# Optimization experiments

Measured on AMD Instinct MI355X. Metric: run time of the kernel, lower is better.

Reference implementation:

```python
import jax, jax.numpy as jnp
import numpy as np

B, T, N, C = 32, 12, 1024, 2   # batch, lookback window, n_series, in_channels
D, H, K, OUT = 16, 64, 2, 12   # embedding_dim, rnn_units, cheb_k, out_dim (horizon)


def setup_inputs() -> dict:
    key = jax.random.key(0)
    ks = jax.random.split(key, 12)
    p = lambda k, sh, s=0.1: jax.random.normal(k, sh, dtype=jnp.float32) * s
    return {
        "source": jax.random.normal(ks[0], (B, T, N, C), dtype=jnp.float32),
        "node_emb": p(ks[1], (N, D), 0.3),
        # layer 0: dim_in = C + H
        "gate_w0": p(ks[2], (D, K, C + H, 2 * H)),
        "gate_b0": p(ks[3], (D, 2 * H)),
        "upd_w0": p(ks[4], (D, K, C + H, H)),
        "upd_b0": p(ks[5], (D, H)),
        # layer 1: dim_in = H + H
        "gate_w1": p(ks[6], (D, K, 2 * H, 2 * H)),
        "gate_b1": p(ks[7], (D, 2 * H)),
        "upd_w1": p(ks[8], (D, K, 2 * H, H)),
        "upd_b1": p(ks[9], (D, H)),
        # end_conv: Conv2d(1, OUT*out_channels, kernel=(1,H)) == linear over hidden dim
        "conv_w": p(ks[10], (OUT, H)),
        "conv_b": p(ks[11], (OUT,)),
    }


def _supports(node_emb):
    # softmax(relu(E E^T)) row-normalized adaptive adjacency; Chebyshev stack (K, N, N)
    A = jax.nn.softmax(jax.nn.relu(node_emb @ node_emb.T), axis=1)
    s = [jnp.eye(N, dtype=A.dtype), A]
    for _ in range(2, K):
        s.append(2.0 * A @ s[-1] - s[-2])
    return jnp.stack(s, axis=0)


def _gcn(x, node_emb, w_pool, b_pool, supports):
    # x: (B, N, Cin); per-node adaptive weights from pools
    w = jnp.einsum('nd,dkio->nkio', node_emb, w_pool)     # (N, K, Cin, Cout)
    b = node_emb @ b_pool                                 # (N, Cout)
    xg = jnp.einsum('knm,bmc->bnkc', supports, x)         # (B, N, K, Cin)
    return jnp.einsum('bnki,nkio->bno', xg, w) + b


def _layer(x_seq, node_emb, supports, gw, gb, uw, ub):
    # x_seq: (B, T, N, Cin) -> (B, T, N, H) via GRU-style AGCRN cell, scanned over T
    def step(state, x_t):
        inp = jnp.concatenate([x_t, state], axis=-1)
        zr = jax.nn.sigmoid(_gcn(inp, node_emb, gw, gb, supports))
        z, r = jnp.split(zr, 2, axis=-1)
        cand = jnp.concatenate([x_t, z * state], axis=-1)
        hc = jnp.tanh(_gcn(cand, node_emb, uw, ub, supports))
        h = r * state + (1.0 - r) * hc
        return h, h

    init = jnp.zeros((x_seq.shape[0], N, H), dtype=x_seq.dtype)
    _, hs = jax.lax.scan(step, init, jnp.swapaxes(x_seq, 0, 1))
    return jnp.swapaxes(hs, 0, 1)


def reference(source, node_emb, gate_w0, gate_b0, upd_w0, upd_b0,
              gate_w1, gate_b1, upd_w1, upd_b1, conv_w, conv_b,
              teacher_forcing_ratio=0):
    sup = _supports(node_emb)  # adaptive supports depend only on static node_emb
    h1 = _layer(source, node_emb, sup, gate_w0, gate_b0, upd_w0, upd_b0)
    h2 = _layer(h1, node_emb, sup, gate_w1, gate_b1, upd_w1, upd_b1)
    last = h2[:, -1]  # (B, N, H)
    # end_conv over hidden dim -> (B, OUT, N); out_channels==1 so squeeze folds away
    out = jnp.einsum('bnh,oh->bon', last, conv_w) + conv_b[None, :, None]
    return out
```

## Files before the change

kernel.cpp:

```cpp
#include <hip/hip_runtime.h>
#include <hip/hip_fp16.h>


typedef _Float16 f16x8 __attribute__((ext_vector_type(8)));
typedef _Float16 f16x4 __attribute__((ext_vector_type(4)));
typedef float f32x4 __attribute__((ext_vector_type(4)));

__global__ __launch_bounds__(256) void compute_A_kernel(const float* __restrict__ E,
                                                        __half* __restrict__ Ah) {
  int n = blockIdx.x;
  int tid = threadIdx.x;
  __shared__ float red[256];
  float en[16];
#pragma unroll
  for (int d = 0; d < 16; ++d) en[d] = E[n * 16 + d];
  float v[4];
#pragma unroll
  for (int q = 0; q < 4; ++q) {
    int m = tid + q * 256;
    const float* Em = E + m * 16;
    float dot = 0.f;
#pragma unroll
    for (int d = 0; d < 16; ++d) dot += en[d] * Em[d];
    v[q] = fmaxf(dot, 0.f);
  }
  float mx = fmaxf(fmaxf(v[0], v[1]), fmaxf(v[2], v[3]));
  red[tid] = mx; __syncthreads();
  for (int s = 128; s > 0; s >>= 1) { if (tid < s) red[tid] = fmaxf(red[tid], red[tid + s]); __syncthreads(); }
  mx = red[0];
  __syncthreads();
  float e[4], sum = 0.f;
#pragma unroll
  for (int q = 0; q < 4; ++q) { e[q] = expf(v[q] - mx); sum += e[q]; }
  red[tid] = sum; __syncthreads();
  for (int s = 128; s > 0; s >>= 1) { if (tid < s) red[tid] += red[tid + s]; __syncthreads(); }
  float inv = 1.f / red[0];
#pragma unroll
  for (int q = 0; q < 4; ++q) Ah[(size_t)n * 1024 + tid + q * 256] = __float2half(e[q] * inv);
}

__global__ void build_e16_kernel(const float* __restrict__ E, __half* __restrict__ E16) {
  int t = blockIdx.x * 256 + threadIdx.x;
  if (t >= 1024 * 32) return;
  int d = t & 31;
  E16[t] = (d < 16) ? __float2half(E[(t >> 5) * 16 + d]) : __half(0);
}

__global__ void pool_t16_kernel(const float* __restrict__ gw0, const float* __restrict__ uw0,
                                const float* __restrict__ gw1, const float* __restrict__ uw1,
                                __half* __restrict__ poolT16) {
  int t = blockIdx.x * 256 + threadIdx.x;
  if (t >= 79872 * 32) return;
  int d = t & 31, j = t >> 5;
  if (d >= 16) { poolT16[t] = __half(0); return; }
  const float* pool; int F, Fp, O, loc;
  if (j < 20480)      { pool = gw0; F = 66;  Fp = 80;  O = 128; loc = j; }
  else if (j < 30720) { pool = uw0; F = 66;  Fp = 80;  O = 64;  loc = j - 20480; }
  else if (j < 63488) { pool = gw1; F = 128; Fp = 128; O = 128; loc = j - 30720; }
  else                { pool = uw1; F = 128; Fp = 128; O = 64;  loc = j - 63488; }
  int KIp = 2 * Fp;
  int o = loc / KIp, kip = loc - o * KIp;
  int kk = (kip >= Fp) ? 1 : 0;
  int jj = kip - kk * Fp;
  int i;
  if (F == Fp) i = jj;
  else i = (jj < 64) ? jj + 2 : (jj < 66 ? jj - 64 : -1);
  poolT16[t] = (i >= 0) ? __float2half(pool[(((size_t)d * 2 + kk) * F + i) * O + o]) : __half(0);
}

__global__ __launch_bounds__(256) void make_wt_mfma_kernel(
    const __half* __restrict__ E16g, const __half* __restrict__ poolT16g,
    __half* __restrict__ WtG0, __half* __restrict__ WtU0,
    __half* __restrict__ WtG1, __half* __restrict__ WtU1) {
  __shared__ __align__(16) _Float16 Es[64][40];
  __shared__ __align__(16) _Float16 wbuf[64][264];
  const _Float16* E16 = (const _Float16*)E16g;
  const _Float16* pT = (const _Float16*)poolT16g;
  int bx = blockIdx.x;
  __half* Wt; int OK, jbase;
  if (bx < 80)       { Wt = WtG0; OK = 128 * 160; jbase = bx * 256; }
  else if (bx < 120) { Wt = WtU0; OK = 64 * 160;  jbase = (bx - 80) * 256; }
  else if (bx < 248) { Wt = WtG1; OK = 128 * 256; jbase = (bx - 120) * 256; }
  else               { Wt = WtU1; OK = 64 * 256;  jbase = (bx - 248) * 256; }
  int jglob0 = bx * 256;
  int n0 = blockIdx.y * 64;
  {
    int r = threadIdx.x >> 2, ch = (threadIdx.x & 3) * 8;
    *(f16x8*)&Es[r][ch] = *(const f16x8*)(E16 + (size_t)(n0 + r) * 32 + ch);
  }
  __syncthreads();
  int wave = threadIdx.x >> 6, lane = threadIdx.x & 63;
  int fm = lane & 15, fg = lane >> 4;
  f16x8 af[4];
#pragma unroll
  for (int i = 0; i < 4; ++i) af[i] = *(const f16x8*)&Es[i * 16 + fm][fg * 8];
  f32x4 acc[4][4] = {};
#pragma unroll
  for (int j = 0; j < 4; ++j) {
    int jc = jglob0 + wave * 64 + j * 16 + fm;
    f16x8 bf = *(const f16x8*)(pT + (size_t)jc * 32 + fg * 8);
#pragma unroll
    for (int i = 0; i < 4; ++i)
      acc[i][j] = __builtin_amdgcn_mfma_f32_16x16x32_f16(af[i], bf, acc[i][j], 0, 0, 0);
  }
#pragma unroll
  for (int i = 0; i < 4; ++i)
#pragma unroll
    for (int j = 0; j < 4; ++j)
#pragma unroll
      for (int r = 0; r < 4; ++r)
        wbuf[i * 16 + fg * 4 + r][wave * 64 + j * 16 + fm] = (_Float16)acc[i][j][r];
  __syncthreads();
  for (int idx = threadIdx.x; idx < 64 * 32; idx += 256) {
    int nsub = idx >> 5, pos = (idx & 31) * 8;
    *(float4*)(Wt + (size_t)(n0 + nsub) * OK + jbase + pos) = *(float4*)&wbuf[nsub][pos];
  }
}

__global__ void make_b_all_kernel(const float* __restrict__ E,
                                  const float* __restrict__ gb0, const float* __restrict__ ub0,
                                  const float* __restrict__ gb1, const float* __restrict__ ub1,
                                  float* __restrict__ Bg0, float* __restrict__ Bu0,
                                  float* __restrict__ Bg1, float* __restrict__ Bu1) {
  int tid = blockIdx.x * 256 + threadIdx.x;
  if (tid >= 1024 * 384) return;
  int n = tid / 384, c = tid - n * 384;
  const float* pool; float* outp; int O, o;
  if (c < 128)      { pool = gb0; outp = Bg0; O = 128; o = c; }
  else if (c < 192) { pool = ub0; outp = Bu0; O = 64;  o = c - 128; }
  else if (c < 320) { pool = gb1; outp = Bg1; O = 128; o = c - 192; }
  else              { pool = ub1; outp = Bu1; O = 64;  o = c - 320; }
  const float* En = E + n * 16;
  float a = 0.f;
#pragma unroll
  for (int d = 0; d < 16; ++d) a += En[d] * pool[d * O + o];
  outp[n * O + o] = a;
}

__global__ void zero_kernel(float* __restrict__ p, int count) {
  int i = blockIdx.x * 256 + threadIdx.x;
  if (i < count) p[i] = 0.f;
}

__global__ void build_x16_kernel(const float* __restrict__ src, __half* __restrict__ x16) {
  int bid = blockIdx.x; int t = bid >> 5, b = bid & 31;
  const float* s = src + (size_t)(b * 12 + t) * 2048;
  __half* dst = x16 + t * 64 + b * 2;
  for (int n = threadIdx.x; n < 1024; n += 256) {
    float2 v = *(const float2*)(s + n * 2);
    *(__half2*)(dst + (size_t)n * 768) = __floats2half2_rn(v.x, v.y);
  }
}

__global__ __launch_bounds__(256) void gemm_nt_kernel(
    const __half* __restrict__ Ahg, const __half* __restrict__ X0g,
    const __half* __restrict__ X1g, __half* __restrict__ Yg,
    int Nc, int cstride, int split) {
  __shared__ __align__(16) _Float16 As[64][136];
  __shared__ __align__(16) _Float16 Bs[64][144];
  const _Float16* __restrict__ Ah = (const _Float16*)Ahg;
  _Float16* __restrict__ Y = (_Float16*)Yg;
  int tid = threadIdx.x;
  int row0 = blockIdx.y * 64;
  int col0 = blockIdx.x * 64;
  const _Float16* __restrict__ Xsrc =
      (col0 < split) ? (const _Float16*)X0g : (const _Float16*)X1g;
  int colg = (col0 < split) ? col0 : col0 - split;
  int wave = tid >> 6, lane = tid & 63;
  int wm = wave & 1, wn = wave >> 1;
  int fm = lane & 15, fg = lane >> 4;

  int sr = tid >> 2, sc = (tid & 3) * 32;
  const _Float16* pa = Ah + (size_t)(row0 + sr) * 1024 + sc;
  int kq = tid & 31, cg = tid >> 5;
  int kb = 4 * kq;
  const _Float16* pb = Xsrc + (size_t)kb * cstride + colg + cg * 8;
  int chunk = kq >> 1;
  int kin = (kq & 1) * 4;

  f16x8 ra[4], rb[4];
#pragma unroll
  for (int c = 0; c < 4; ++c) ra[c] = *(const f16x8*)(pa + c * 8);
#pragma unroll
  for (int r = 0; r < 4; ++r) rb[r] = *(const f16x8*)(pb + (size_t)r * cstride);

  f32x4 acc[2][2] = {};
  for (int k0 = 0; k0 < 1024; k0 += 128) {
#pragma unroll
    for (int c = 0; c < 4; ++c) *(f16x8*)&As[sr][sc + c * 8] = ra[c];
#pragma unroll
    for (int i = 0; i < 8; ++i) {
      int c = cg * 8 + i;
      f16x4 p;
      p[0] = rb[0][i]; p[1] = rb[1][i]; p[2] = rb[2][i]; p[3] = rb[3][i];
      *(f16x4*)&Bs[c][((chunk ^ (c & 7)) << 3) + kin] = p;
    }
    __syncthreads();
    if (k0 + 128 < 1024) {
#pragma unroll
      for (int c = 0; c < 4; ++c) ra[c] = *(const f16x8*)(pa + k0 + 128 + c * 8);
#pragma unroll
      for (int r = 0; r < 4; ++r)
        rb[r] = *(const f16x8*)(pb + (size_t)(k0 + 128 + r) * cstride);
    }
#pragma unroll
    for (int kc = 0; kc < 4; ++kc) {
      int ck = kc * 4 + fg;
      f16x8 af[2], bf[2];
#pragma unroll
      for (int i = 0; i < 2; ++i)
        af[i] = *(const f16x8*)&As[wm * 32 + i * 16 + fm][kc * 32 + fg * 8];
#pragma unroll
      for (int j = 0; j < 2; ++j) {
        int cl = wn * 32 + j * 16 + fm;
        bf[j] = *(const f16x8*)&Bs[cl][(ck ^ (cl & 7)) << 3];
      }
#pragma unroll
      for (int i = 0; i < 2; ++i)
#pragma unroll
        for (int j = 0; j < 2; ++j)
          acc[i][j] = __builtin_amdgcn_mfma_f32_16x16x32_f16(af[i], bf[j], acc[i][j], 0, 0, 0);
    }
    __syncthreads();
  }
#pragma unroll
  for (int i = 0; i < 2; ++i) {
#pragma unroll
    for (int j = 0; j < 2; ++j) {
      int col = col0 + wn * 32 + j * 16 + fm;
      int rbase = row0 + wm * 32 + i * 16 + fg * 4;
#pragma unroll
      for (int r = 0; r < 4; ++r)
        Y[(size_t)(rbase + r) * Nc + col] = (_Float16)acc[i][j][r];
    }
  }
}

__global__ __launch_bounds__(256) void gate0_kernel(
    const __half* __restrict__ h16, const __half* __restrict__ YB,
    const float* __restrict__ src, const __half* __restrict__ Axt, int tstep,
    const __half* __restrict__ Wtg, const float* __restrict__ Bg,
    const float* __restrict__ h32, __half* __restrict__ zh, float* __restrict__ rbuf) {
  constexpr int KIP = 160, STRIDE = 168;
  __shared__ __align__(16) _Float16 Xs[32 * STRIDE];
  int n = blockIdx.x;
  int t = threadIdx.x;
#pragma unroll
  for (int u = 0; u < 2; ++u) {
    int idx = t + u * 256;
    int b = idx >> 4, part = (idx >> 3) & 1, ch = idx & 7;
    const _Float16* s = part ? (const _Float16*)YB + (size_t)n * 2048 + b * 64 + ch * 8
                             : (const _Float16*)h16 + (size_t)n * 2048 + b * 64 + ch * 8;
    *(f16x8*)&Xs[b * STRIDE + part * 80 + ch * 8] = *(const f16x8*)s;
  }
  if (t < 32) {
    int b = t;
    float2 xv = *(const float2*)(src + ((size_t)(b * 12 + tstep) * 1024 + n) * 2);
    Xs[b * STRIDE + 64] = (_Float16)xv.x;
    Xs[b * STRIDE + 65] = (_Float16)xv.y;
    const _Float16* ax = (const _Float16*)Axt + (size_t)n * 768 + tstep * 64 + b * 2;
    Xs[b * STRIDE + 144] = ax[0];
    Xs[b * STRIDE + 145] = ax[1];
  }
  for (int idx = t; idx < 896; idx += 256) {
    int b = idx / 28, jj = idx % 28;
    int col = (jj < 14) ? 66 + jj : 132 + jj;
    Xs[b * STRIDE + col] = (_Float16)0.f;
  }
  __syncthreads();
  int wave = t >> 6, lane = t & 63;
  int fm = lane & 15, fg = lane >> 4;
  f32x4 acc[2][2] = {};
  const _Float16* Wn = (const _Float16*)Wtg + ((size_t)n * 128 + wave * 32) * KIP;
#pragma unroll
  for (int kc = 0; kc < KIP / 32; ++kc) {
    f16x8 af[2], bf[2];
#pragma unroll
    for (int i = 0; i < 2; ++i)
      af[i] = *(const f16x8*)&Xs[(i * 16 + fm) * STRIDE + kc * 32 + fg * 8];
#pragma unroll
    for (int j = 0; j < 2; ++j)
      bf[j] = *(const f16x8*)(Wn + (size_t)(j * 16 + fm) * KIP + kc * 32 + fg * 8);
#pragma unroll
    for (int i = 0; i < 2; ++i)
#pragma unroll
      for (int j = 0; j < 2; ++j)
        acc[i][j] = __builtin_amdgcn_mfma_f32_16x16x32_f16(af[i], bf[j], acc[i][j], 0, 0, 0);
  }
  const float* Bn = Bg + n * 128;
#pragma unroll
  for (int j = 0; j < 2; ++j) {
    int o = wave * 32 + j * 16 + fm;
    float bias = Bn[o];
#pragma unroll
    for (int i = 0; i < 2; ++i)
#pragma unroll
      for (int r = 0; r < 4; ++r) {
        int b = i * 16 + fg * 4 + r;
        float s = 1.f / (1.f + __expf(-(acc[i][j][r] + bias)));
        size_t base = (size_t)n * 2048 + b * 64;
        if (o < 64) zh[base + o] = __float2half(s * h32[base + o]);
        else        rbuf[base + o - 64] = s;
      }
  }
}

__global__ __launch_bounds__(256) void upd0_kernel(
    const __half* __restrict__ zh, const __half* __restrict__ YA2,
    const float* __restrict__ src, const __half* __restrict__ Axt, int tstep,
    const __half* __restrict__ Wtg, const float* __restrict__ Bu,
    const float* __restrict__ rbuf, float* __restrict__ h32, __half* __restrict__ h16) {
  constexpr int KIP = 160, STRIDE = 168;
  __shared__ __align__(16) _Float16 Xs[32 * STRIDE];
  int n = blockIdx.x;
  int t = threadIdx.x;
#pragma unroll
  for (int u = 0; u < 2; ++u) {
    int idx = t + u * 256;
    int b = idx >> 4, part = (idx >> 3) & 1, ch = idx & 7;
    const _Float16* s = part ? (const _Float16*)YA2 + (size_t)n * 4096 + b * 64 + ch * 8
                             : (const _Float16*)zh + (size_t)n * 2048 + b * 64 + ch * 8;
    *(f16x8*)&Xs[b * STRIDE + part * 80 + ch * 8] = *(const f16x8*)s;
  }
  if (t < 32) {
    int b = t;
    float2 xv = *(const float2*)(src + ((size_t)(b * 12 + tstep) * 1024 + n) * 2);
    Xs[b * STRIDE + 64] = (_Float16)xv.x;
    Xs[b * STRIDE + 65] = (_Float16)xv.y;
    const _Float16* ax = (const _Float16*)Axt + (size_t)n * 768 + tstep * 64 + b * 2;
    Xs[b * STRIDE + 144] = ax[0];
    Xs[b * STRIDE + 145] = ax[1];
  }
  for (int idx = t; idx < 896; idx += 256) {
    int b = idx / 28, jj = idx % 28;
    int col = (jj < 14) ? 66 + jj : 132 + jj;
    Xs[b * STRIDE + col] = (_Float16)0.f;
  }
  __syncthreads();
  int wave = t >> 6, lane = t & 63;
  int fm = lane & 15, fg = lane >> 4;
  f32x4 acc[2] = {};
  const _Float16* Wn = (const _Float16*)Wtg + ((size_t)n * 64 + wave * 16) * KIP;
#pragma unroll
  for (int kc = 0; kc < KIP / 32; ++kc) {
    f16x8 bf = *(const f16x8*)(Wn + (size_t)fm * KIP + kc * 32 + fg * 8);
#pragma unroll
    for (int i = 0; i < 2; ++i) {
      f16x8 af = *(const f16x8*)&Xs[(i * 16 + fm) * STRIDE + kc * 32 + fg * 8];
      acc[i] = __builtin_amdgcn_mfma_f32_16x16x32_f16(af, bf, acc[i], 0, 0, 0);
    }
  }
  int o = wave * 16 + fm;
  float bias = Bu[n * 64 + o];
#pragma unroll
  for (int i = 0; i < 2; ++i)
#pragma unroll
    for (int r = 0; r < 4; ++r) {
      int b = i * 16 + fg * 4 + r;
      float x = acc[i][r] + bias;
      x = fminf(fmaxf(x, -15.f), 15.f);
      float e = __expf(2.f * x);
      float hc = (e - 1.f) / (e + 1.f);
      size_t base = (size_t)n * 2048 + b * 64;
      float rr = rbuf[base + o];
      float hnew = rr * h32[base + o] + (1.f - rr) * hc;
      h32[base + o] = hnew;
      h16[base + o] = __float2half(hnew);
    }
}

__global__ __launch_bounds__(256) void gate1_kernel(
    const __half* __restrict__ h1_16, const __half* __restrict__ h2_16,
    const __half* __restrict__ YB, const __half* __restrict__ YA2,
    const __half* __restrict__ Wtg, const float* __restrict__ Bg,
    const float* __restrict__ h32, __half* __restrict__ zh, float* __restrict__ rbuf) {
  constexpr int KIP = 256, STRIDE = 264;
  __shared__ __align__(16) _Float16 Xs[32 * STRIDE];
  int n = blockIdx.x;
  int t = threadIdx.x;
#pragma unroll
  for (int u = 0; u < 4; ++u) {
    int idx = t + u * 256;
    int b = idx >> 5, q = idx & 31;
    const _Float16* s;
    if (q < 8)       s = (const _Float16*)h1_16 + (size_t)n * 2048 + b * 64 + q * 8;
    else if (q < 16) s = (const _Float16*)h2_16 + (size_t)n * 2048 + b * 64 + (q - 8) * 8;
    else if (q < 24) s = (const _Float16*)YB + (size_t)n * 2048 + b * 64 + (q - 16) * 8;
    else             s = (const _Float16*)YA2 + (size_t)n * 4096 + 2048 + b * 64 + (q - 24) * 8;
    *(f16x8*)&Xs[b * STRIDE + q * 8] = *(const f16x8*)s;
  }
  __syncthreads();
  int wave = t >> 6, lane = t & 63;
  int fm = lane & 15, fg = lane >> 4;
  f32x4 acc[2][2] = {};
  const _Float16* Wn = (const _Float16*)Wtg + ((size_t)n * 128 + wave * 32) * KIP;
#pragma unroll
  for (int kc = 0; kc < KIP / 32; ++kc) {
    f16x8 af[2], bf[2];
#pragma unroll
    for (int i = 0; i < 2; ++i)
      af[i] = *(const f16x8*)&Xs[(i * 16 + fm) * STRIDE + kc * 32 + fg * 8];
#pragma unroll
    for (int j = 0; j < 2; ++j)
      bf[j] = *(const f16x8*)(Wn + (size_t)(j * 16 + fm) * KIP + kc * 32 + fg * 8);
#pragma unroll
    for (int i = 0; i < 2; ++i)
#pragma unroll
      for (int j = 0; j < 2; ++j)
        acc[i][j] = __builtin_amdgcn_mfma_f32_16x16x32_f16(af[i], bf[j], acc[i][j], 0, 0, 0);
  }
  const float* Bn = Bg + n * 128;
#pragma unroll
  for (int j = 0; j < 2; ++j) {
    int o = wave * 32 + j * 16 + fm;
    float bias = Bn[o];
#pragma unroll
    for (int i = 0; i < 2; ++i)
#pragma unroll
      for (int r = 0; r < 4; ++r) {
        int b = i * 16 + fg * 4 + r;
        float s = 1.f / (1.f + __expf(-(acc[i][j][r] + bias)));
        size_t base = (size_t)n * 2048 + b * 64;
        if (o < 64) zh[base + o] = __float2half(s * h32[base + o]);
        else        rbuf[base + o - 64] = s;
      }
  }
}

__global__ __launch_bounds__(256) void upd1_kernel(
    const __half* __restrict__ h1_16, const __half* __restrict__ zh,
    const __half* __restrict__ YB, const __half* __restrict__ YC,
    const __half* __restrict__ Wtg, const float* __restrict__ Bu,
    const float* __restrict__ rbuf, float* __restrict__ h32, __half* __restrict__ h16) {
  constexpr int KIP = 256, STRIDE = 264;
  __shared__ __align__(16) _Float16 Xs[32 * STRIDE];
  int n = blockIdx.x;
  int t = threadIdx.x;
#pragma unroll
  for (int u = 0; u < 4; ++u) {
    int idx = t + u * 256;
    int b = idx >> 5, q = idx & 31;
    const _Float16* s;
    if (q < 8)       s = (const _Float16*)h1_16 + (size_t)n * 2048 + b * 64 + q * 8;
    else if (q < 16) s = (const _Float16*)zh + (size_t)n * 2048 + b * 64 + (q - 8) * 8;
    else if (q < 24) s = (const _Float16*)YB + (size_t)n * 2048 + b * 64 + (q - 16) * 8;
    else             s = (const _Float16*)YC + (size_t)n * 2048 + b * 64 + (q - 24) * 8;
    *(f16x8*)&Xs[b * STRIDE + q * 8] = *(const f16x8*)s;
  }
  __syncthreads();
  int wave = t >> 6, lane = t & 63;
  int fm = lane & 15, fg = lane >> 4;
  f32x4 acc[2] = {};
  const _Float16* Wn = (const _Float16*)Wtg + ((size_t)n * 64 + wave * 16) * KIP;
#pragma unroll
  for (int kc = 0; kc < KIP / 32; ++kc) {
    f16x8 bf = *(const f16x8*)(Wn + (size_t)fm * KIP + kc * 32 + fg * 8);
#pragma unroll
    for (int i = 0; i < 2; ++i) {
      f16x8 af = *(const f16x8*)&Xs[(i * 16 + fm) * STRIDE + kc * 32 + fg * 8];
      acc[i] = __builtin_amdgcn_mfma_f32_16x16x32_f16(af, bf, acc[i], 0, 0, 0);
    }
  }
  int o = wave * 16 + fm;
  float bias = Bu[n * 64 + o];
#pragma unroll
  for (int i = 0; i < 2; ++i)
#pragma unroll
    for (int r = 0; r < 4; ++r) {
      int b = i * 16 + fg * 4 + r;
      float x = acc[i][r] + bias;
      x = fminf(fmaxf(x, -15.f), 15.f);
      float e = __expf(2.f * x);
      float hc = (e - 1.f) / (e + 1.f);
      size_t base = (size_t)n * 2048 + b * 64;
      float rr = rbuf[base + o];
      float hnew = rr * h32[base + o] + (1.f - rr) * hc;
      h32[base + o] = hnew;
      h16[base + o] = __float2half(hnew);
    }
}

__global__ void final_conv_kernel(const float* __restrict__ h2, const float* __restrict__ cw,
                                  const float* __restrict__ cb, float* __restrict__ out) {
  int tid = blockIdx.x * 256 + threadIdx.x;
  if (tid >= 32 * 1024) return;
  int n = tid & 1023, b = tid >> 10;
  const float* hp = h2 + ((size_t)n * 32 + b) * 64;
  float hv[64];
#pragma unroll
  for (int i = 0; i < 64; ++i) hv[i] = hp[i];
#pragma unroll
  for (int o = 0; o < 12; ++o) {
    float acc = cb[o];
#pragma unroll
    for (int i = 0; i < 64; ++i) acc += hv[i] * cw[o * 64 + i];
    out[((size_t)b * 12 + o) * 1024 + n] = acc;
  }
}

extern "C" void kernel_launch(void* const* d_in, const int* in_sizes, int n_in,
                              void* d_out, int out_size, void* d_ws, size_t ws_size,
                              hipStream_t stream) {
  const float* src = (const float*)d_in[0];
  const float* E   = (const float*)d_in[1];
  const float* gw0 = (const float*)d_in[2];
  const float* gb0 = (const float*)d_in[3];
  const float* uw0 = (const float*)d_in[4];
  const float* ub0 = (const float*)d_in[5];
  const float* gw1 = (const float*)d_in[6];
  const float* gb1 = (const float*)d_in[7];
  const float* uw1 = (const float*)d_in[8];
  const float* ub1 = (const float*)d_in[9];
  const float* cw  = (const float*)d_in[10];
  const float* cb  = (const float*)d_in[11];
  float* out = (float*)d_out;
  (void)in_sizes; (void)n_in; (void)out_size; (void)ws_size;

  char* base = (char*)d_ws;
  size_t off = 0;
  auto alloc = [&](size_t bytes) -> void* {
    void* p = base + off; off += (bytes + 511) & ~(size_t)511; return p;
  };
  __half* Ah   = (__half*)alloc((size_t)1024 * 1024 * 2);
  __half* WtG0 = (__half*)alloc((size_t)1024 * 128 * 160 * 2);
  __half* WtU0 = (__half*)alloc((size_t)1024 * 64 * 160 * 2);
  __half* WtG1 = (__half*)alloc((size_t)1024 * 128 * 256 * 2);
  __half* WtU1 = (__half*)alloc((size_t)1024 * 64 * 256 * 2);
  float*  Bg0  = (float*) alloc((size_t)1024 * 128 * 4);
  float*  Bu0  = (float*) alloc((size_t)1024 * 64 * 4);
  float*  Bg1  = (float*) alloc((size_t)1024 * 128 * 4);
  float*  Bu1  = (float*) alloc((size_t)1024 * 64 * 4);
  float*  h1_32 = (float*)alloc((size_t)1024 * 2048 * 4);
  float*  h2_32 = (float*)alloc((size_t)1024 * 2048 * 4);
  __half* h1_16 = (__half*)alloc((size_t)1024 * 2048 * 2);
  __half* h2_16 = (__half*)alloc((size_t)1024 * 2048 * 2);
  __half* YB   = (__half*)alloc((size_t)1024 * 2048 * 2);
  __half* zh   = (__half*)alloc((size_t)1024 * 2048 * 2);
  __half* YA2  = (__half*)alloc((size_t)1024 * 4096 * 2);
  __half* YC   = (__half*)alloc((size_t)1024 * 2048 * 2);
  __half* Axt  = (__half*)alloc((size_t)1024 * 768 * 2);
  float*  rbuf = (float*) alloc((size_t)1024 * 2048 * 4);
  __half* poolT16 = (__half*)rbuf;
  __half* E16  = poolT16 + (size_t)79872 * 32;
  __half* x16  = E16 + (size_t)1024 * 32;

  compute_A_kernel<<<1024, 256, 0, stream>>>(E, Ah);
  build_e16_kernel<<<(1024 * 32 + 255) / 256, 256, 0, stream>>>(E, E16);
  pool_t16_kernel<<<(79872 * 32 + 255) / 256, 256, 0, stream>>>(gw0, uw0, gw1, uw1, poolT16);
  make_wt_mfma_kernel<<<dim3(312, 16), 256, 0, stream>>>(E16, poolT16, WtG0, WtU0, WtG1, WtU1);
  make_b_all_kernel<<<(1024 * 384 + 255) / 256, 256, 0, stream>>>(E, gb0, ub0, gb1, ub1,
                                                                  Bg0, Bu0, Bg1, Bu1);
  build_x16_kernel<<<384, 256, 0, stream>>>(src, x16);
  gemm_nt_kernel<<<dim3(12, 16), 256, 0, stream>>>(Ah, (__half*)x16, (__half*)x16, Axt,
                                                   768, 768, 768);
  zero_kernel<<<(7340032 + 255) / 256, 256, 0, stream>>>(h1_32, 7340032);

  for (int t = 0; t < 12; ++t) {
    gate0_kernel<<<1024, 256, 0, stream>>>(h1_16, YB, src, Axt, t, WtG0, Bg0, h1_32, zh, rbuf);
    gemm_nt_kernel<<<dim3(64, 16), 256, 0, stream>>>(Ah, zh, h2_16, YA2, 4096, 2048, 2048);
    upd0_kernel<<<1024, 256, 0, stream>>>(zh, YA2, src, Axt, t, WtU0, Bu0, rbuf, h1_32, h1_16);
    gemm_nt_kernel<<<dim3(32, 16), 256, 0, stream>>>(Ah, h1_16, h1_16, YB, 2048, 2048, 2048);
    gate1_kernel<<<1024, 256, 0, stream>>>(h1_16, h2_16, YB, YA2, WtG1, Bg1, h2_32, zh, rbuf);
    gemm_nt_kernel<<<dim3(32, 16), 256, 0, stream>>>(Ah, zh, zh, YC, 2048, 2048, 2048);
    upd1_kernel<<<1024, 256, 0, stream>>>(h1_16, zh, YB, YC, WtU1, Bu1, rbuf, h2_32, h2_16);
  }

  final_conv_kernel<<<(32 * 1024 + 255) / 256, 256, 0, stream>>>(h2_32, cw, cb, out);
}
```

Measured before the change: 1.516 ms.

## Fuse next-step layer-0 gate into layer-1 update; add 64x128-tile support GEMM

Layer-0's gate computation for step t+1 now runs inside the layer-1 update kernel of step t. This drops one kernel launch per timestep and reuses the per-node block's shared memory. Separate zh/r buffers are introduced for the two layers so the fused gate cannot clobber state that is still in use. The large 4096-column support GEMM now uses a new kernel with 64x128 tiles, a register prefetch of the next K slice and a swizzled B layout in LDS, halving the grid. The trade-off is higher register and LDS pressure per block, plus extra buffers.

```diff
diff --git a/kernel.cpp b/kernel.cpp
--- a/kernel.cpp
+++ b/kernel.cpp
@@ -236,15 +236,103 @@
   }
 }
 
-__global__ __launch_bounds__(256) void gate0_kernel(
+__global__ __launch_bounds__(256) void gemm_nt128_kernel(
+    const __half* __restrict__ Ahg, const __half* __restrict__ X0g,
+    const __half* __restrict__ X1g, __half* __restrict__ Yg,
+    int Nc, int cstride, int split) {
+  __shared__ __align__(16) _Float16 As[64][136];
+  __shared__ __align__(16) _Float16 Bs[128][144];
+  const _Float16* __restrict__ Ah = (const _Float16*)Ahg;
+  _Float16* __restrict__ Y = (_Float16*)Yg;
+  int tid = threadIdx.x;
+  int row0 = blockIdx.y * 64;
+  int col0 = blockIdx.x * 128;
+  const _Float16* __restrict__ Xsrc =
+      (col0 < split) ? (const _Float16*)X0g : (const _Float16*)X1g;
+  int colg = (col0 < split) ? col0 : col0 - split;
+  int wave = tid >> 6, lane = tid & 63;
+  int fm = lane & 15, fg = lane >> 4;
+
+  int sr = tid >> 2, sc = (tid & 3) * 32;
+  const _Float16* pa = Ah + (size_t)(row0 + sr) * 1024 + sc;
+  int kq = tid & 31, cg = tid >> 5;
+  int kb = 4 * kq;
+  const _Float16* pb = Xsrc + (size_t)kb * cstride + colg + cg * 16;
+  int chunk = kq >> 1;
+  int kin = (kq & 1) * 4;
+
+  f16x8 ra[4], rb[4][2];
+#pragma unroll
+  for (int c = 0; c < 4; ++c) ra[c] = *(const f16x8*)(pa + c * 8);
+#pragma unroll
+  for (int r = 0; r < 4; ++r)
+#pragma unroll
+    for (int h = 0; h < 2; ++h)
+      rb[r][h] = *(const f16x8*)(pb + (size_t)r * cstride + h * 8);
+
+  f32x4 acc[4][2] = {};
+  for (int k0 = 0; k0 < 1024; k0 += 128) {
+#pragma unroll
+    for (int c = 0; c < 4; ++c) *(f16x8*)&As[sr][sc + c * 8] = ra[c];
+#pragma unroll
+    for (int h = 0; h < 2; ++h)
+#pragma unroll
+      for (int i = 0; i < 8; ++i) {
+        int c = cg * 16 + h * 8 + i;
+        f16x4 p;
+        p[0] = rb[0][h][i]; p[1] = rb[1][h][i]; p[2] = rb[2][h][i]; p[3] = rb[3][h][i];
+        *(f16x4*)&Bs[c][((chunk ^ (c & 7)) << 3) + kin] = p;
+      }
+    __syncthreads();
+    if (k0 + 128 < 1024) {
+#pragma unroll
+      for (int c = 0; c < 4; ++c) ra[c] = *(const f16x8*)(pa + k0 + 128 + c * 8);
+#pragma unroll
+      for (int r = 0; r < 4; ++r)
+#pragma unroll
+        for (int h = 0; h < 2; ++h)
+          rb[r][h] = *(const f16x8*)(pb + (size_t)(k0 + 128 + r) * cstride + h * 8);
+    }
+#pragma unroll
+    for (int kc = 0; kc < 4; ++kc) {
+      int ck = kc * 4 + fg;
+      f16x8 af[4], bf[2];
+#pragma unroll
+      for (int i = 0; i < 4; ++i)
+        af[i] = *(const f16x8*)&As[i * 16 + fm][kc * 32 + fg * 8];
+#pragma unroll
+      for (int j = 0; j < 2; ++j) {
+        int cl = wave * 32 + j * 16 + fm;
+        bf[j] = *(const f16x8*)&Bs[cl][(ck ^ (cl & 7)) << 3];
+      }
+#pragma unroll
+      for (int i = 0; i < 4; ++i)
+#pragma unroll
+        for (int j = 0; j < 2; ++j)
+          acc[i][j] = __builtin_amdgcn_mfma_f32_16x16x32_f16(af[i], bf[j], acc[i][j], 0, 0, 0);
+    }
+    __syncthreads();
+  }
+#pragma unroll
+  for (int i = 0; i < 4; ++i) {
+#pragma unroll
+    for (int j = 0; j < 2; ++j) {
+      int col = col0 + wave * 32 + j * 16 + fm;
+      int rbase = row0 + i * 16 + fg * 4;
+#pragma unroll
+      for (int r = 0; r < 4; ++r)
+        Y[(size_t)(rbase + r) * Nc + col] = (_Float16)acc[i][j][r];
+    }
+  }
+}
+
+__device__ __forceinline__ void gate0_body(
+    _Float16* Xs, int n, int t,
     const __half* __restrict__ h16, const __half* __restrict__ YB,
     const float* __restrict__ src, const __half* __restrict__ Axt, int tstep,
     const __half* __restrict__ Wtg, const float* __restrict__ Bg,
-    const float* __restrict__ h32, __half* __restrict__ zh, float* __restrict__ rbuf) {
+    const float* __restrict__ h32, __half* __restrict__ zh0, float* __restrict__ r0) {
   constexpr int KIP = 160, STRIDE = 168;
-  __shared__ __align__(16) _Float16 Xs[32 * STRIDE];
-  int n = blockIdx.x;
-  int t = threadIdx.x;
 #pragma unroll
   for (int u = 0; u < 2; ++u) {
     int idx = t + u * 256;
@@ -299,17 +387,26 @@
         int b = i * 16 + fg * 4 + r;
         float s = 1.f / (1.f + __expf(-(acc[i][j][r] + bias)));
         size_t base = (size_t)n * 2048 + b * 64;
-        if (o < 64) zh[base + o] = __float2half(s * h32[base + o]);
-        else        rbuf[base + o - 64] = s;
+        if (o < 64) zh0[base + o] = __float2half(s * h32[base + o]);
+        else        r0[base + o - 64] = s;
       }
   }
 }
 
+__global__ __launch_bounds__(256) void gate0_kernel(
+    const __half* __restrict__ h16, const __half* __restrict__ YB,
+    const float* __restrict__ src, const __half* __restrict__ Axt, int tstep,
+    const __half* __restrict__ Wtg, const float* __restrict__ Bg,
+    const float* __restrict__ h32, __half* __restrict__ zh0, float* __restrict__ r0) {
+  __shared__ __align__(16) _Float16 Xs[32 * 168];
+  gate0_body(Xs, blockIdx.x, threadIdx.x, h16, YB, src, Axt, tstep, Wtg, Bg, h32, zh0, r0);
+}
+
 __global__ __launch_bounds__(256) void upd0_kernel(
-    const __half* __restrict__ zh, const __half* __restrict__ YA2,
+    const __half* __restrict__ zh0, const __half* __restrict__ YA2,
     const float* __restrict__ src, const __half* __restrict__ Axt, int tstep,
     const __half* __restrict__ Wtg, const float* __restrict__ Bu,
-    const float* __restrict__ rbuf, float* __restrict__ h32, __half* __restrict__ h16) {
+    const float* __restrict__ r0, float* __restrict__ h32, __half* __restrict__ h16) {
   constexpr int KIP = 160, STRIDE = 168;
   __shared__ __align__(16) _Float16 Xs[32 * STRIDE];
   int n = blockIdx.x;
@@ -319,7 +416,7 @@
     int idx = t + u * 256;
     int b = idx >> 4, part = (idx >> 3) & 1, ch = idx & 7;
     const _Float16* s = part ? (const _Float16*)YA2 + (size_t)n * 4096 + b * 64 + ch * 8
-                             : (const _Float16*)zh + (size_t)n * 2048 + b * 64 + ch * 8;
+                             : (const _Float16*)zh0 + (size_t)n * 2048 + b * 64 + ch * 8;
     *(f16x8*)&Xs[b * STRIDE + part * 80 + ch * 8] = *(const f16x8*)s;
   }
   if (t < 32) {
@@ -362,7 +459,7 @@
       float e = __expf(2.f * x);
       float hc = (e - 1.f) / (e + 1.f);
       size_t base = (size_t)n * 2048 + b * 64;
-      float rr = rbuf[base + o];
+      float rr = r0[base + o];
       float hnew = rr * h32[base + o] + (1.f - rr) * hc;
       h32[base + o] = hnew;
       h16[base + o] = __float2half(hnew);
@@ -373,7 +470,7 @@
     const __half* __restrict__ h1_16, const __half* __restrict__ h2_16,
     const __half* __restrict__ YB, const __half* __restrict__ YA2,
     const __half* __restrict__ Wtg, const float* __restrict__ Bg,
-    const float* __restrict__ h32, __half* __restrict__ zh, float* __restrict__ rbuf) {
+    const float* __restrict__ h32, __half* __restrict__ zh1, float* __restrict__ r1) {
   constexpr int KIP = 256, STRIDE = 264;
   __shared__ __align__(16) _Float16 Xs[32 * STRIDE];
   int n = blockIdx.x;
@@ -421,17 +518,21 @@
         int b = i * 16 + fg * 4 + r;
         float s = 1.f / (1.f + __expf(-(acc[i][j][r] + bias)));
         size_t base = (size_t)n * 2048 + b * 64;
-        if (o < 64) zh[base + o] = __float2half(s * h32[base + o]);
-        else        rbuf[base + o - 64] = s;
+        if (o < 64) zh1[base + o] = __float2half(s * h32[base + o]);
+        else        r1[base + o - 64] = s;
       }
   }
 }
 
-__global__ __launch_bounds__(256) void upd1_kernel(
-    const __half* __restrict__ h1_16, const __half* __restrict__ zh,
+__global__ __launch_bounds__(256) void upd1_gate0_kernel(
+    const __half* __restrict__ h1_16, const __half* __restrict__ zh1,
     const __half* __restrict__ YB, const __half* __restrict__ YC,
-    const __half* __restrict__ Wtg, const float* __restrict__ Bu,
-    const float* __restrict__ rbuf, float* __restrict__ h32, __half* __restrict__ h16) {
+    const __half* __restrict__ WtU1, const float* __restrict__ Bu1,
+    const float* __restrict__ r1, float* __restrict__ h2_32, __half* __restrict__ h2_16,
+    const float* __restrict__ src, const __half* __restrict__ Axt, int tnext,
+    const __half* __restrict__ WtG0, const float* __restrict__ Bg0,
+    const float* __restrict__ h1_32, __half* __restrict__ zh0, float* __restrict__ r0,
+    int do_gate0) {
   constexpr int KIP = 256, STRIDE = 264;
   __shared__ __align__(16) _Float16 Xs[32 * STRIDE];
   int n = blockIdx.x;
@@ -442,7 +543,7 @@
     int b = idx >> 5, q = idx & 31;
     const _Float16* s;
     if (q < 8)       s = (const _Float16*)h1_16 + (size_t)n * 2048 + b * 64 + q * 8;
-    else if (q < 16) s = (const _Float16*)zh + (size_t)n * 2048 + b * 64 + (q - 8) * 8;
+    else if (q < 16) s = (const _Float16*)zh1 + (size_t)n * 2048 + b * 64 + (q - 8) * 8;
     else if (q < 24) s = (const _Float16*)YB + (size_t)n * 2048 + b * 64 + (q - 16) * 8;
     else             s = (const _Float16*)YC + (size_t)n * 2048 + b * 64 + (q - 24) * 8;
     *(f16x8*)&Xs[b * STRIDE + q * 8] = *(const f16x8*)s;
@@ -450,34 +551,39 @@
   __syncthreads();
   int wave = t >> 6, lane = t & 63;
   int fm = lane & 15, fg = lane >> 4;
-  f32x4 acc[2] = {};
-  const _Float16* Wn = (const _Float16*)Wtg + ((size_t)n * 64 + wave * 16) * KIP;
-#pragma unroll
-  for (int kc = 0; kc < KIP / 32; ++kc) {
-    f16x8 bf = *(const f16x8*)(Wn + (size_t)fm * KIP + kc * 32 + fg * 8);
-#pragma unroll
-    for (int i = 0; i < 2; ++i) {
-      f16x8 af = *(const f16x8*)&Xs[(i * 16 + fm) * STRIDE + kc * 32 + fg * 8];
-      acc[i] = __builtin_amdgcn_mfma_f32_16x16x32_f16(af, bf, acc[i], 0, 0, 0);
-    }
-  }
-  int o = wave * 16 + fm;
-  float bias = Bu[n * 64 + o];
-#pragma unroll
-  for (int i = 0; i < 2; ++i)
-#pragma unroll
-    for (int r = 0; r < 4; ++r) {
-      int b = i * 16 + fg * 4 + r;
-      float x = acc[i][r] + bias;
-      x = fminf(fmaxf(x, -15.f), 15.f);
-      float e = __expf(2.f * x);
-      float hc = (e - 1.f) / (e + 1.f);
-      size_t base = (size_t)n * 2048 + b * 64;
-      float rr = rbuf[base + o];
-      float hnew = rr * h32[base + o] + (1.f - rr) * hc;
-      h32[base + o] = hnew;
-      h16[base + o] = __float2half(hnew);
-    }
+  {
+    f32x4 acc[2] = {};
+    const _Float16* Wn = (const _Float16*)WtU1 + ((size_t)n * 64 + wave * 16) * KIP;
+#pragma unroll
+    for (int kc = 0; kc < KIP / 32; ++kc) {
+      f16x8 bf = *(const f16x8*)(Wn + (size_t)fm * KIP + kc * 32 + fg * 8);
+#pragma unroll
+      for (int i = 0; i < 2; ++i) {
+        f16x8 af = *(const f16x8*)&Xs[(i * 16 + fm) * STRIDE + kc * 32 + fg * 8];
+        acc[i] = __builtin_amdgcn_mfma_f32_16x16x32_f16(af, bf, acc[i], 0, 0, 0);
+      }
+    }
+    int o = wave * 16 + fm;
+    float bias = Bu1[n * 64 + o];
+#pragma unroll
+    for (int i = 0; i < 2; ++i)
+#pragma unroll
+      for (int r = 0; r < 4; ++r) {
+        int b = i * 16 + fg * 4 + r;
+        float x = acc[i][r] + bias;
+        x = fminf(fmaxf(x, -15.f), 15.f);
+        float e = __expf(2.f * x);
+        float hc = (e - 1.f) / (e + 1.f);
+        size_t base = (size_t)n * 2048 + b * 64;
+        float rr = r1[base + o];
+        float hnew = rr * h2_32[base + o] + (1.f - rr) * hc;
+        h2_32[base + o] = hnew;
+        h2_16[base + o] = __float2half(hnew);
+      }
+  }
+  if (!do_gate0) return;
+  __syncthreads();
+  gate0_body(Xs, n, t, h1_16, YB, src, Axt, tnext, WtG0, Bg0, h1_32, zh0, r0);
 }
 
 __global__ void final_conv_kernel(const float* __restrict__ h2, const float* __restrict__ cw,
@@ -535,12 +641,14 @@
   __half* h1_16 = (__half*)alloc((size_t)1024 * 2048 * 2);
   __half* h2_16 = (__half*)alloc((size_t)1024 * 2048 * 2);
   __half* YB   = (__half*)alloc((size_t)1024 * 2048 * 2);
-  __half* zh   = (__half*)alloc((size_t)1024 * 2048 * 2);
+  __half* zh0  = (__half*)alloc((size_t)1024 * 2048 * 2);
+  __half* zh1  = (__half*)alloc((size_t)1024 * 2048 * 2);
   __half* YA2  = (__half*)alloc((size_t)1024 * 4096 * 2);
   __half* YC   = (__half*)alloc((size_t)1024 * 2048 * 2);
   __half* Axt  = (__half*)alloc((size_t)1024 * 768 * 2);
-  float*  rbuf = (float*) alloc((size_t)1024 * 2048 * 4);
-  __half* poolT16 = (__half*)rbuf;
+  float*  r1   = (float*) alloc((size_t)1024 * 2048 * 4);
+  float*  r0   = (float*) alloc((size_t)1024 * 2048 * 4);
+  __half* poolT16 = (__half*)r0;
   __half* E16  = poolT16 + (size_t)79872 * 32;
   __half* x16  = E16 + (size_t)1024 * 32;
 
@@ -554,15 +662,17 @@
   gemm_nt_kernel<<<dim3(12, 16), 256, 0, stream>>>(Ah, (__half*)x16, (__half*)x16, Axt,
                                                    768, 768, 768);
   zero_kernel<<<(7340032 + 255) / 256, 256, 0, stream>>>(h1_32, 7340032);
+  gate0_kernel<<<1024, 256, 0, stream>>>(h1_16, YB, src, Axt, 0, WtG0, Bg0, h1_32, zh0, r0);
 
   for (int t = 0; t < 12; ++t) {
-    gate0_kernel<<<1024, 256, 0, stream>>>(h1_16, YB, src, Axt, t, WtG0, Bg0, h1_32, zh, rbuf);
-    gemm_nt_kernel<<<dim3(64, 16), 256, 0, stream>>>(Ah, zh, h2_16, YA2, 4096, 2048, 2048);
-    upd0_kernel<<<1024, 256, 0, stream>>>(zh, YA2, src, Axt, t, WtU0, Bu0, rbuf, h1_32, h1_16);
+    gemm_nt128_kernel<<<dim3(32, 16), 256, 0, stream>>>(Ah, zh0, h2_16, YA2, 4096, 2048, 2048);
+    upd0_kernel<<<1024, 256, 0, stream>>>(zh0, YA2, src, Axt, t, WtU0, Bu0, r0, h1_32, h1_16);
     gemm_nt_kernel<<<dim3(32, 16), 256, 0, stream>>>(Ah, h1_16, h1_16, YB, 2048, 2048, 2048);
-    gate1_kernel<<<1024, 256, 0, stream>>>(h1_16, h2_16, YB, YA2, WtG1, Bg1, h2_32, zh, rbuf);
-    gemm_nt_kernel<<<dim3(32, 16), 256, 0, stream>>>(Ah, zh, zh, YC, 2048, 2048, 2048);
-    upd1_kernel<<<1024, 256, 0, stream>>>(h1_16, zh, YB, YC, WtU1, Bu1, rbuf, h2_32, h2_16);
+    gate1_kernel<<<1024, 256, 0, stream>>>(h1_16, h2_16, YB, YA2, WtG1, Bg1, h2_32, zh1, r1);
+    gemm_nt_kernel<<<dim3(32, 16), 256, 0, stream>>>(Ah, zh1, zh1, YC, 2048, 2048, 2048);
+    upd1_gate0_kernel<<<1024, 256, 0, stream>>>(h1_16, zh1, YB, YC, WtU1, Bu1, r1, h2_32, h2_16,
+                                                src, Axt, t + 1, WtG0, Bg0, h1_32, zh0, r0,
+                                                (t < 11) ? 1 : 0);
   }
 
   final_conv_kernel<<<(32 * 1024 + 255) / 256, 256, 0, stream>>>(h2_32, cw, cb, out);
```

Result: faster. 1.446 ms (-4.6%).
